# Performance work log

Hardware: AMD Instinct MI355X
Metric: run time of the kernel (lower is better)

Reference implementation:

```python
import jax, jax.numpy as jnp
import numpy as np

B, N, D, H, PD, HID = 16, 512, 512, 8, 9, 32
DH = D // H


def setup_inputs() -> dict:
    key = jax.random.key(0)
    ks = jax.random.split(key, 8)
    h = jax.random.normal(ks[0], (B, N, D), dtype=jnp.float32)
    v = jax.random.normal(ks[1], (B, N, 4), dtype=jnp.float32)
    m = jax.random.randint(ks[2], (B, N), 0, 2, dtype=jnp.int32)
    token_type_ids = jax.random.randint(ks[3], (N,), 0, 4, dtype=jnp.int32)
    s = 1.0 / np.sqrt(D)
    W_qkv = jax.random.normal(ks[4], (D, 3 * D), dtype=jnp.float32) * s
    W_out = jax.random.normal(ks[5], (D, D), dtype=jnp.float32) * s
    W1 = jax.random.normal(ks[6], (PD, HID), dtype=jnp.float32) * (1.0 / np.sqrt(PD))
    b1 = jnp.zeros((HID,), dtype=jnp.float32)
    W2 = jax.random.normal(ks[7], (HID, H), dtype=jnp.float32) * (1.0 / np.sqrt(HID))
    b2 = jnp.zeros((H,), dtype=jnp.float32)
    return {"h": h, "v": v, "m": m, "token_type_ids": token_type_ids,
            "W_qkv": W_qkv, "W_out": W_out, "W1": W1, "b1": b1, "W2": W2, "b2": b2}


def build_pairwise_features(v, token_type_ids):
    # v: [B,N,4] -> e: [B,N,N,9] = [v_i - v_j (4), v_i * v_j (4), same_type (1)]
    vi = v[:, :, None, :]
    vj = v[:, None, :, :]
    same = (token_type_ids[:, None] == token_type_ids[None, :]).astype(v.dtype)
    same = jnp.broadcast_to(same[None, :, :, None], v.shape[:1] + same.shape + (1,))
    return jnp.concatenate([vi - vj, vi * vj, same], axis=-1)


def reference(h, v, m, token_type_ids, W_qkv, W_out, W1, b1, W2, b2):
    Bq, Nq, Dq = h.shape
    qkv = h @ W_qkv                                    # [B,N,3D]
    q, k, vv = jnp.split(qkv, 3, axis=-1)
    def heads(x):
        return x.reshape(Bq, Nq, H, DH).transpose(0, 2, 1, 3)  # [B,H,N,dh]
    q, k, vv = heads(q), heads(k), heads(vv)
    logits = jnp.einsum('bhid,bhjd->bhij', q, k) / jnp.sqrt(jnp.float32(DH))
    e = build_pairwise_features(v, token_type_ids)     # [B,N,N,9]
    bias = jax.nn.relu(e @ W1 + b1) @ W2 + b2          # [B,N,N,H]
    logits = logits + bias.transpose(0, 3, 1, 2)       # [B,H,N,N]
    key_invalid = (m == 0)[:, None, None, :]           # [B,1,1,N]
    logits = jnp.where(key_invalid, -jnp.inf, logits)
    attn = jax.nn.softmax(logits, axis=-1)             # dropout is identity (p=0/eval)
    out = jnp.einsum('bhij,bhjd->bhid', attn, vv)
    out = out.transpose(0, 2, 1, 3).reshape(Bq, Nq, Dq) @ W_out
    out = out * (m != 0).astype(out.dtype)[:, :, None]
    return out
```

## Files before the change

### kernel.cpp

```cpp
#include <hip/hip_runtime.h>
#include <hip/hip_bf16.h>
#include <hip/hip_fp16.h>

#define NN 512
#define HH 8
#define DHH 64

typedef __attribute__((ext_vector_type(8))) short short8v;
typedef __attribute__((ext_vector_type(8))) unsigned short ushort8v;
typedef __attribute__((ext_vector_type(4))) unsigned short ushort4v;
typedef __attribute__((ext_vector_type(4))) float f32x4;
typedef __attribute__((ext_vector_type(8))) _Float16 f16x8;
typedef __attribute__((ext_vector_type(4))) _Float16 f16x4;

__device__ __forceinline__ unsigned short f2bf(float x) {
  unsigned u = __builtin_bit_cast(unsigned, x);
  u += 0x7FFFu + ((u >> 16) & 1u);
  return (unsigned short)(u >> 16);
}
__device__ __forceinline__ int swz64(int r, int cb) { return r * 64 + (cb ^ (((r >> 1) & 3) << 4)); }
__device__ __forceinline__ int swz128(int r, int cb) { return r * 128 + (cb ^ ((r & 7) << 4)); }

__global__ __launch_bounds__(256) void cvt_bf(const float* __restrict__ src,
                                              unsigned short* __restrict__ dst, int n) {
  int i = (blockIdx.x * 256 + threadIdx.x) * 4;
  if (i < n) {
    float4 v = *(const float4*)&src[i];
    ushort4v o;
    o[0] = f2bf(v.x); o[1] = f2bf(v.y); o[2] = f2bf(v.z); o[3] = f2bf(v.w);
    *(ushort4v*)&dst[i] = o;
  }
}

__global__ __launch_bounds__(256) void transpose_cvt(const float* __restrict__ src,
                                                     unsigned short* __restrict__ dst,
                                                     int R, int C) {
  __shared__ float t[32][33];
  const int r0 = blockIdx.x * 32, c0 = blockIdx.y * 32;
  const int rr = threadIdx.x >> 3, c4 = (threadIdx.x & 7) * 4;
  float4 v = *(const float4*)&src[(size_t)(r0 + rr) * C + c0 + c4];
  t[rr][c4 + 0] = v.x; t[rr][c4 + 1] = v.y; t[rr][c4 + 2] = v.z; t[rr][c4 + 3] = v.w;
  __syncthreads();
  ushort4v o;
#pragma unroll
  for (int e = 0; e < 4; ++e) o[e] = f2bf(t[c4 + e][rr]);
  *(ushort4v*)&dst[(size_t)(c0 + rr) * R + r0 + c4] = o;
}

__device__ __forceinline__ void gemm128_body(const unsigned short* __restrict__ A,
                                             const unsigned short* __restrict__ Bt,
                                             int ldk, int m0, int n0,
                                             f32x4 acc[4][4], unsigned char* smem) {
  const int tid = threadIdx.x, lane = tid & 63, wid = tid >> 6;
  const int wm = wid >> 1, wn = wid & 1;
  int aoff[4], boff[4];
#pragma unroll
  for (int i = 0; i < 4; ++i) {
    aoff[i] = swz64(wm * 64 + i * 16 + (lane & 15), (lane >> 4) * 16);
    boff[i] = 8192 + swz64(wn * 64 + i * 16 + (lane & 15), (lane >> 4) * 16);
  }
  for (int k0 = 0; k0 < ldk; k0 += 32) {
#pragma unroll
    for (int p = 0; p < 2; ++p) {
      const int idx = p * 256 + tid;
      const int r = idx >> 2, cg = idx & 3;
      ushort8v av = *(const ushort8v*)&A[(size_t)(m0 + r) * ldk + k0 + cg * 8];
      *(ushort8v*)&smem[swz64(r, cg * 16)] = av;
      ushort8v bv = *(const ushort8v*)&Bt[(size_t)(n0 + r) * ldk + k0 + cg * 8];
      *(ushort8v*)&smem[8192 + swz64(r, cg * 16)] = bv;
    }
    __syncthreads();
    short8v a[4], b[4];
#pragma unroll
    for (int i = 0; i < 4; ++i) {
      a[i] = *(const short8v*)&smem[aoff[i]];
      b[i] = *(const short8v*)&smem[boff[i]];
    }
#pragma unroll
    for (int i = 0; i < 4; ++i)
#pragma unroll
      for (int j = 0; j < 4; ++j)
        acc[i][j] = __builtin_amdgcn_mfma_f32_16x16x32_bf16(a[i], b[j], acc[i][j], 0, 0, 0);
    __syncthreads();
  }
}

__global__ __launch_bounds__(256) void gemm_qkv(const unsigned short* __restrict__ A,
                                                const unsigned short* __restrict__ Bt,
                                                unsigned short* __restrict__ q,
                                                unsigned short* __restrict__ k,
                                                unsigned short* __restrict__ vt) {
  __shared__ unsigned char smem[16384];
  f32x4 acc[4][4];
  const f32x4 z = {0.f, 0.f, 0.f, 0.f};
#pragma unroll
  for (int i = 0; i < 4; ++i)
#pragma unroll
    for (int j = 0; j < 4; ++j) acc[i][j] = z;
  gemm128_body(A, Bt, 512, blockIdx.x * 128, blockIdx.y * 128, acc, smem);
  const int lane = threadIdx.x & 63, wid = threadIdx.x >> 6;
  const int wm = wid >> 1, wn = wid & 1;
#pragma unroll
  for (int i = 0; i < 4; ++i) {
    const int row0 = blockIdx.x * 128 + wm * 64 + i * 16 + ((lane >> 4) << 2);
#pragma unroll
    for (int j = 0; j < 4; ++j) {
      const int col = blockIdx.y * 128 + wn * 64 + j * 16 + (lane & 15);
      const int part = col >> 9, head = (col >> 6) & 7, dh = col & 63;
#pragma unroll
      for (int rr = 0; rr < 4; ++rr) {
        const int row = row0 + rr;
        const int b_ = row >> 9, n_ = row & 511;
        const unsigned short val = f2bf(acc[i][j][rr]);
        if (part == 0)
          q[(((b_ * HH + head) * NN) + n_) * DHH + dh] = val;
        else if (part == 1)
          k[(((b_ * HH + head) * NN) + n_) * DHH + dh] = val;
        else
          vt[(((b_ * HH + head) * DHH) + dh) * NN + n_] = val;
      }
    }
  }
}

__global__ __launch_bounds__(256) void gemm_out(const unsigned short* __restrict__ A,
                                                const unsigned short* __restrict__ Bt,
                                                const int* __restrict__ msk,
                                                float* __restrict__ out) {
  __shared__ unsigned char smem[16384];
  f32x4 acc[4][4];
  const f32x4 z = {0.f, 0.f, 0.f, 0.f};
#pragma unroll
  for (int i = 0; i < 4; ++i)
#pragma unroll
    for (int j = 0; j < 4; ++j) acc[i][j] = z;
  gemm128_body(A, Bt, 512, blockIdx.x * 128, blockIdx.y * 128, acc, smem);
  const int lane = threadIdx.x & 63, wid = threadIdx.x >> 6;
  const int wm = wid >> 1, wn = wid & 1;
#pragma unroll
  for (int i = 0; i < 4; ++i) {
    const int row0 = blockIdx.x * 128 + wm * 64 + i * 16 + ((lane >> 4) << 2);
#pragma unroll
    for (int j = 0; j < 4; ++j) {
      const int col = blockIdx.y * 128 + wn * 64 + j * 16 + (lane & 15);
#pragma unroll
      for (int rr = 0; rr < 4; ++rr) {
        const int row = row0 + rr;
        const float mm = (msk[row] != 0) ? 1.f : 0.f;
        out[(size_t)row * 512 + col] = acc[i][j][rr] * mm;
      }
    }
  }
}

__global__ __launch_bounds__(512, 4) void attn_bias_fused(
    const unsigned short* __restrict__ q, const unsigned short* __restrict__ k,
    const unsigned short* __restrict__ vt, const float* __restrict__ vvec,
    const int* __restrict__ tti, const int* __restrict__ msk,
    const float* __restrict__ W1, const float* __restrict__ b1,
    const float* __restrict__ W2, const float* __restrict__ b2,
    unsigned short* __restrict__ ao) {
  __shared__ float sv[NN][4];
  __shared__ int stt[NN];
  __shared__ float smask[NN];
  __shared__ _Float16 bias_lds[2][HH][16][68];
  __shared__ _Float16 hbuf[HH][16 * 40];
  __shared__ unsigned char ps[HH][2048];
  const int tid = threadIdx.x, lane = tid & 63, w = tid >> 6;
  const int l16 = lane & 15, lg = lane >> 4;
  const int it = blockIdx.x, b_ = blockIdx.y;
  const int i0 = it * 16;
  for (int idx = tid; idx < NN; idx += 512) {
    *(float4*)&sv[idx][0] = *(const float4*)&vvec[(b_ * NN + idx) * 4];
    stt[idx] = tti[idx];
    smask[idx] = (msk[b_ * NN + idx] != 0) ? 0.f : -1e30f;
  }
  f16x8 w1f[2], w2f;
#pragma unroll
  for (int t = 0; t < 2; ++t)
#pragma unroll
    for (int e = 0; e < 8; ++e) {
      const int kk = lg * 8 + e;
      w1f[t][e] = (kk < 9) ? (_Float16)W1[kk * 32 + t * 16 + l16] : (_Float16)0.f;
    }
#pragma unroll
  for (int e = 0; e < 8; ++e)
    w2f[e] = (l16 < 8) ? (_Float16)W2[(lg * 8 + e) * 8 + l16] : (_Float16)0.f;
  const float b1v0 = b1[l16], b1v1 = b1[16 + l16];
  const float b2v = (l16 < 8) ? b2[l16] : 0.f;
  const unsigned short* qb = q + ((size_t)(b_ * HH + w) * NN + i0) * DHH;
  const unsigned short* kb = k + (size_t)(b_ * HH + w) * NN * DHH;
  const unsigned short* vtb = vt + (size_t)(b_ * HH + w) * DHH * NN;
  short8v qf[2];
#pragma unroll
  for (int kc = 0; kc < 2; ++kc)
    qf[kc] = *(const short8v*)&qb[l16 * DHH + kc * 32 + lg * 8];
  f32x4 acc[4];
  const f32x4 z = {0.f, 0.f, 0.f, 0.f};
#pragma unroll
  for (int d = 0; d < 4; ++d) acc[d] = z;
  float mrow[4], lrow[4];
#pragma unroll
  for (int r = 0; r < 4; ++r) { mrow[r] = -1e30f; lrow[r] = 0.f; }
  _Float16* hb = &hbuf[w][0];
  __syncthreads();
  int pbuf = 0;
  for (int j0 = 0; j0 < NN; j0 += 64) {
    for (int tt = 0; tt < 8; ++tt) {
      const int il = w * 2 + (tt >> 2), jg = tt & 3;
      const float4 vi = *(const float4*)&sv[i0 + il][0];
      const int ti = stt[i0 + il];
      const int j = j0 + jg * 16 + l16;
      const float4 vj = *(const float4*)&sv[j][0];
      f16x8 af = {0, 0, 0, 0, 0, 0, 0, 0};
      if (lg == 0) {
        af[0] = (_Float16)(vi.x - vj.x); af[1] = (_Float16)(vi.y - vj.y);
        af[2] = (_Float16)(vi.z - vj.z); af[3] = (_Float16)(vi.w - vj.w);
        af[4] = (_Float16)(vi.x * vj.x); af[5] = (_Float16)(vi.y * vj.y);
        af[6] = (_Float16)(vi.z * vj.z); af[7] = (_Float16)(vi.w * vj.w);
      } else if (lg == 1) {
        af[0] = (ti == stt[j]) ? (_Float16)1.f : (_Float16)0.f;
      }
      f32x4 h0 = {b1v0, b1v0, b1v0, b1v0};
      f32x4 h1 = {b1v1, b1v1, b1v1, b1v1};
      h0 = __builtin_amdgcn_mfma_f32_16x16x32_f16(af, w1f[0], h0, 0, 0, 0);
      h1 = __builtin_amdgcn_mfma_f32_16x16x32_f16(af, w1f[1], h1, 0, 0, 0);
#pragma unroll
      for (int r = 0; r < 4; ++r) {
        const int row = lg * 4 + r;
        hb[row * 40 + l16] = (_Float16)fmaxf(h0[r], 0.f);
        hb[row * 40 + 16 + l16] = (_Float16)fmaxf(h1[r], 0.f);
      }
      f16x8 af2 = *(const f16x8*)&hb[l16 * 40 + lg * 8];
      f32x4 o = {b2v, b2v, b2v, b2v};
      o = __builtin_amdgcn_mfma_f32_16x16x32_f16(af2, w2f, o, 0, 0, 0);
      if (l16 < 8) {
        f16x4 pk;
#pragma unroll
        for (int r = 0; r < 4; ++r) pk[r] = (_Float16)o[r];
        *(f16x4*)&bias_lds[pbuf][l16][il][jg * 16 + lg * 4] = pk;
      }
    }
    __syncthreads();
    f32x4 s[4];
#pragma unroll
    for (int jt = 0; jt < 4; ++jt) {
      const unsigned short* kr = &kb[(j0 + jt * 16 + l16) * DHH + lg * 8];
      short8v kf0 = *(const short8v*)&kr[0];
      short8v kf1 = *(const short8v*)&kr[32];
      f32x4 t = z;
      t = __builtin_amdgcn_mfma_f32_16x16x32_bf16(qf[0], kf0, t, 0, 0, 0);
      t = __builtin_amdgcn_mfma_f32_16x16x32_bf16(qf[1], kf1, t, 0, 0, 0);
      s[jt] = t;
    }
#pragma unroll
    for (int jt = 0; jt < 4; ++jt) {
      const int jcol = j0 + jt * 16 + l16;
      const float mk = smask[jcol];
#pragma unroll
      for (int r = 0; r < 4; ++r) {
        const float bv = (float)bias_lds[pbuf][w][lg * 4 + r][jt * 16 + l16];
        s[jt][r] = fmaf(s[jt][r], 0.125f, bv) + mk;
      }
    }
    float alpha[4];
#pragma unroll
    for (int r = 0; r < 4; ++r) {
      float tm = fmaxf(fmaxf(s[0][r], s[1][r]), fmaxf(s[2][r], s[3][r]));
      tm = fmaxf(tm, __shfl_xor(tm, 1));
      tm = fmaxf(tm, __shfl_xor(tm, 2));
      tm = fmaxf(tm, __shfl_xor(tm, 4));
      tm = fmaxf(tm, __shfl_xor(tm, 8));
      const float mn = fmaxf(mrow[r], tm);
      alpha[r] = __expf(mrow[r] - mn);
      mrow[r] = mn;
      float ts = 0.f;
#pragma unroll
      for (int jt = 0; jt < 4; ++jt) {
        const float p = __expf(s[jt][r] - mn);
        s[jt][r] = p;
        ts += p;
      }
      ts += __shfl_xor(ts, 1);
      ts += __shfl_xor(ts, 2);
      ts += __shfl_xor(ts, 4);
      ts += __shfl_xor(ts, 8);
      lrow[r] = lrow[r] * alpha[r] + ts;
    }
#pragma unroll
    for (int d = 0; d < 4; ++d)
#pragma unroll
      for (int r = 0; r < 4; ++r) acc[d][r] *= alpha[r];
#pragma unroll
    for (int jt = 0; jt < 4; ++jt)
#pragma unroll
      for (int r = 0; r < 4; ++r)
        *(unsigned short*)&ps[w][swz128(lg * 4 + r, jt * 32 + 2 * l16)] = f2bf(s[jt][r]);
    short8v pf[2];
#pragma unroll
    for (int kc = 0; kc < 2; ++kc)
      pf[kc] = *(const short8v*)&ps[w][swz128(l16, kc * 64 + lg * 16)];
#pragma unroll
    for (int d = 0; d < 4; ++d) {
      const unsigned short* vr = &vtb[(size_t)(d * 16 + l16) * NN + j0 + lg * 8];
      short8v vf0 = *(const short8v*)&vr[0];
      short8v vf1 = *(const short8v*)&vr[32];
      acc[d] = __builtin_amdgcn_mfma_f32_16x16x32_bf16(pf[0], vf0, acc[d], 0, 0, 0);
      acc[d] = __builtin_amdgcn_mfma_f32_16x16x32_bf16(pf[1], vf1, acc[d], 0, 0, 0);
    }
    pbuf ^= 1;
  }
#pragma unroll
  for (int d = 0; d < 4; ++d) {
#pragma unroll
    for (int r = 0; r < 4; ++r) {
      const int row = i0 + lg * 4 + r;
      ao[(size_t)(b_ * NN + row) * 512 + w * DHH + d * 16 + l16] =
          f2bf(acc[d][r] / lrow[r]);
    }
  }
}

extern "C" void kernel_launch(void* const* d_in, const int* in_sizes, int n_in,
                              void* d_out, int out_size, void* d_ws, size_t ws_size,
                              hipStream_t stream) {
  const float* h     = (const float*)d_in[0];
  const float* v     = (const float*)d_in[1];
  const int*   m     = (const int*)d_in[2];
  const int*   tti   = (const int*)d_in[3];
  const float* W_qkv = (const float*)d_in[4];
  const float* W_out = (const float*)d_in[5];
  const float* W1    = (const float*)d_in[6];
  const float* b1    = (const float*)d_in[7];
  const float* W2    = (const float*)d_in[8];
  const float* b2    = (const float*)d_in[9];
  float* out = (float*)d_out;
  unsigned char* ws = (unsigned char*)d_ws;

  unsigned short* h_bf  = (unsigned short*)(ws + 0);
  unsigned short* q_bf  = (unsigned short*)(ws + 8388608);
  unsigned short* k_bf  = (unsigned short*)(ws + 16777216);
  unsigned short* vt_bf = (unsigned short*)(ws + 25165824);
  unsigned short* ao_bf = (unsigned short*)(ws + 33554432);
  unsigned short* WqT   = (unsigned short*)(ws + 41943040);
  unsigned short* WoT   = (unsigned short*)(ws + 43515904);

  cvt_bf<<<4096, 256, 0, stream>>>(h, h_bf, 16 * NN * 512);
  transpose_cvt<<<dim3(16, 48), 256, 0, stream>>>(W_qkv, WqT, 512, 1536);
  transpose_cvt<<<dim3(16, 16), 256, 0, stream>>>(W_out, WoT, 512, 512);
  gemm_qkv<<<dim3(64, 12), 256, 0, stream>>>(h_bf, WqT, q_bf, k_bf, vt_bf);
  attn_bias_fused<<<dim3(32, 16), 512, 0, stream>>>(q_bf, k_bf, vt_bf, v, tti, m,
                                                    W1, b1, W2, b2, ao_bf);
  gemm_out<<<dim3(64, 4), 256, 0, stream>>>(ao_bf, WoT, m, out);
}
```

Baseline: 154.3 us.

## Shrink attention LDS footprint, swizzle bias buffer, vectorize V-transpose stores

Replaces the double-buffered bias LDS array with a single swizzled buffer and adds a second barrier per tile to protect it. The hidden-layer scratch and the probability scratch now share one per-wave buffer. The aim is to cut LDS usage so more blocks fit per CU, and to reduce bank conflicts on bias reads. The query-row features are hoisted out of the tile loop, the inner loop is unrolled, and the V-transposed output of the QKV GEMM is written as packed 4-element vector stores; the cost is an extra __syncthreads per iteration.

```diff
diff --git a/kernel.cpp b/kernel.cpp
--- a/kernel.cpp
+++ b/kernel.cpp
@@ -11,7 +11,6 @@
 typedef __attribute__((ext_vector_type(4))) unsigned short ushort4v;
 typedef __attribute__((ext_vector_type(4))) float f32x4;
 typedef __attribute__((ext_vector_type(8))) _Float16 f16x8;
-typedef __attribute__((ext_vector_type(4))) _Float16 f16x4;
 
 __device__ __forceinline__ unsigned short f2bf(float x) {
   unsigned u = __builtin_bit_cast(unsigned, x);
@@ -107,17 +106,20 @@
     for (int j = 0; j < 4; ++j) {
       const int col = blockIdx.y * 128 + wn * 64 + j * 16 + (lane & 15);
       const int part = col >> 9, head = (col >> 6) & 7, dh = col & 63;
-#pragma unroll
-      for (int rr = 0; rr < 4; ++rr) {
-        const int row = row0 + rr;
-        const int b_ = row >> 9, n_ = row & 511;
-        const unsigned short val = f2bf(acc[i][j][rr]);
-        if (part == 0)
-          q[(((b_ * HH + head) * NN) + n_) * DHH + dh] = val;
-        else if (part == 1)
-          k[(((b_ * HH + head) * NN) + n_) * DHH + dh] = val;
-        else
-          vt[(((b_ * HH + head) * DHH) + dh) * NN + n_] = val;
+      if (part == 2) {
+        const int b_ = row0 >> 9, n_ = row0 & 511;
+        ushort4v pk;
+#pragma unroll
+        for (int rr = 0; rr < 4; ++rr) pk[rr] = f2bf(acc[i][j][rr]);
+        *(ushort4v*)&vt[(((b_ * HH + head) * DHH) + dh) * NN + n_] = pk;
+      } else {
+        unsigned short* dst = (part == 0) ? q : k;
+#pragma unroll
+        for (int rr = 0; rr < 4; ++rr) {
+          const int row = row0 + rr;
+          const int b_ = row >> 9, n_ = row & 511;
+          dst[(((b_ * HH + head) * NN) + n_) * DHH + dh] = f2bf(acc[i][j][rr]);
+        }
       }
     }
   }
@@ -160,18 +162,17 @@
     const float* __restrict__ W1, const float* __restrict__ b1,
     const float* __restrict__ W2, const float* __restrict__ b2,
     unsigned short* __restrict__ ao) {
-  __shared__ float sv[NN][4];
+  __shared__ float4 sv4[NN];
   __shared__ int stt[NN];
   __shared__ float smask[NN];
-  __shared__ _Float16 bias_lds[2][HH][16][68];
-  __shared__ _Float16 hbuf[HH][16 * 40];
-  __shared__ unsigned char ps[HH][2048];
+  __shared__ unsigned short bias_lds[16 * 512];
+  __shared__ unsigned char wavebuf[HH][2048];
   const int tid = threadIdx.x, lane = tid & 63, w = tid >> 6;
   const int l16 = lane & 15, lg = lane >> 4;
   const int it = blockIdx.x, b_ = blockIdx.y;
   const int i0 = it * 16;
   for (int idx = tid; idx < NN; idx += 512) {
-    *(float4*)&sv[idx][0] = *(const float4*)&vvec[(b_ * NN + idx) * 4];
+    sv4[idx] = *(const float4*)&vvec[(b_ * NN + idx) * 4];
     stt[idx] = tti[idx];
     smask[idx] = (msk[b_ * NN + idx] != 0) ? 0.f : -1e30f;
   }
@@ -202,16 +203,21 @@
   float mrow[4], lrow[4];
 #pragma unroll
   for (int r = 0; r < 4; ++r) { mrow[r] = -1e30f; lrow[r] = 0.f; }
-  _Float16* hb = &hbuf[w][0];
+  _Float16* hb = (_Float16*)&wavebuf[w][0];
+  unsigned char* ps = &wavebuf[w][0];
   __syncthreads();
-  int pbuf = 0;
+  const float4 vi_a = sv4[i0 + w * 2], vi_b = sv4[i0 + w * 2 + 1];
+  const int ti_a = stt[i0 + w * 2], ti_b = stt[i0 + w * 2 + 1];
   for (int j0 = 0; j0 < NN; j0 += 64) {
+#pragma unroll
     for (int tt = 0; tt < 8; ++tt) {
-      const int il = w * 2 + (tt >> 2), jg = tt & 3;
-      const float4 vi = *(const float4*)&sv[i0 + il][0];
-      const int ti = stt[i0 + il];
+      const int jg = tt & 3;
+      const int sec = tt >> 2;
+      const float4 vi = sec ? vi_b : vi_a;
+      const int ti = sec ? ti_b : ti_a;
+      const int il = w * 2 + sec;
       const int j = j0 + jg * 16 + l16;
-      const float4 vj = *(const float4*)&sv[j][0];
+      const float4 vj = sv4[j];
       f16x8 af = {0, 0, 0, 0, 0, 0, 0, 0};
       if (lg == 0) {
         af[0] = (_Float16)(vi.x - vj.x); af[1] = (_Float16)(vi.y - vj.y);
@@ -235,10 +241,14 @@
       f32x4 o = {b2v, b2v, b2v, b2v};
       o = __builtin_amdgcn_mfma_f32_16x16x32_f16(af2, w2f, o, 0, 0, 0);
       if (l16 < 8) {
-        f16x4 pk;
-#pragma unroll
-        for (int r = 0; r < 4; ++r) pk[r] = (_Float16)o[r];
-        *(f16x4*)&bias_lds[pbuf][l16][il][jg * 16 + lg * 4] = pk;
+        const int K2 = (il >> 2) << 1;
+        const int base = il * 512;
+#pragma unroll
+        for (int r = 0; r < 4; ++r) {
+          const int jrel = jg * 16 + lg * 4 + r;
+          bias_lds[base + ((jrel * 8 + l16) ^ K2)] =
+              __builtin_bit_cast(unsigned short, (_Float16)o[r]);
+        }
       }
     }
     __syncthreads();
@@ -253,16 +263,19 @@
       t = __builtin_amdgcn_mfma_f32_16x16x32_bf16(qf[1], kf1, t, 0, 0, 0);
       s[jt] = t;
     }
+    const int K2b = lg << 1;
 #pragma unroll
     for (int jt = 0; jt < 4; ++jt) {
-      const int jcol = j0 + jt * 16 + l16;
-      const float mk = smask[jcol];
+      const int jrel = jt * 16 + l16;
+      const float mk = smask[j0 + jrel];
 #pragma unroll
       for (int r = 0; r < 4; ++r) {
-        const float bv = (float)bias_lds[pbuf][w][lg * 4 + r][jt * 16 + l16];
+        const unsigned short raw = bias_lds[(lg * 4 + r) * 512 + ((jrel * 8 + w) ^ K2b)];
+        const float bv = (float)__builtin_bit_cast(_Float16, raw);
         s[jt][r] = fmaf(s[jt][r], 0.125f, bv) + mk;
       }
     }
+    __syncthreads();
     float alpha[4];
 #pragma unroll
     for (int r = 0; r < 4; ++r) {
@@ -295,11 +308,11 @@
     for (int jt = 0; jt < 4; ++jt)
 #pragma unroll
       for (int r = 0; r < 4; ++r)
-        *(unsigned short*)&ps[w][swz128(lg * 4 + r, jt * 32 + 2 * l16)] = f2bf(s[jt][r]);
+        *(unsigned short*)&ps[swz128(lg * 4 + r, jt * 32 + 2 * l16)] = f2bf(s[jt][r]);
     short8v pf[2];
 #pragma unroll
     for (int kc = 0; kc < 2; ++kc)
-      pf[kc] = *(const short8v*)&ps[w][swz128(l16, kc * 64 + lg * 16)];
+      pf[kc] = *(const short8v*)&ps[swz128(l16, kc * 64 + lg * 16)];
 #pragma unroll
     for (int d = 0; d < 4; ++d) {
       const unsigned short* vr = &vtb[(size_t)(d * 16 + l16) * NN + j0 + lg * 8];
@@ -308,7 +321,6 @@
       acc[d] = __builtin_amdgcn_mfma_f32_16x16x32_bf16(pf[0], vf0, acc[d], 0, 0, 0);
       acc[d] = __builtin_amdgcn_mfma_f32_16x16x32_bf16(pf[1], vf1, acc[d], 0, 0, 0);
     }
-    pbuf ^= 1;
   }
 #pragma unroll
   for (int d = 0; d < 4; ++d) {
```

New measurement: 233.2 us. 1.51x slower.
